# Kernel optimization log

Measured on AMD Instinct MI355X. Metric: run time of the kernel, lower is better.

The kernel has to match this reference:

```python
import jax, jax.numpy as jnp
import numpy as np

B, T, C, H = 8, 1024, 768, 12
D = C // H  # head_dim = 64


def setup_inputs() -> dict:
    key = jax.random.key(0)
    ks = jax.random.split(key, 5)
    return {
        "x": jax.random.normal(ks[0], (B, T, C), dtype=jnp.float32),
        "W_in": jax.random.normal(ks[1], (C, 3 * C), dtype=jnp.float32) * 0.02,
        "b_in": jax.random.normal(ks[2], (3 * C,), dtype=jnp.float32) * 0.02,
        "W_out": jax.random.normal(ks[3], (C, C), dtype=jnp.float32) * 0.02,
        "b_out": jax.random.normal(ks[4], (C,), dtype=jnp.float32) * 0.02,
    }


def reference(x, W_in, b_in, W_out, b_out):
    b, t, c = x.shape
    qkv = x @ W_in + b_in                       # [b, t, 3c]
    # NOTE: original code splits as (k, q, v) -- k first!
    k, q, v = jnp.split(qkv, 3, axis=2)
    # [b, h, t, d]
    k = k.reshape(b, t, H, D).transpose(0, 2, 1, 3)
    q = q.reshape(b, t, H, D).transpose(0, 2, 1, 3)
    v = v.reshape(b, t, H, D).transpose(0, 2, 1, 3)
    # NOTE: original applies NO 1/sqrt(d) scaling.
    scores = jnp.einsum("bhqd,bhkd->bhqk", q, k)
    causal = jnp.tril(jnp.ones((t, t), dtype=bool))
    scores = jnp.where(causal[None, None], scores, -jnp.inf)
    attn = jax.nn.softmax(scores, axis=-1)
    y = jnp.einsum("bhqk,bhkd->bhqd", attn, v)  # [b, h, t, d]
    y = y.transpose(0, 2, 1, 3).reshape(b, t, c)
    return y @ W_out + b_out
```

## Files before the change

kernel.cpp:

```cpp
#include <hip/hip_runtime.h>
#include <hip/hip_bf16.h>
#include <stdint.h>


typedef __bf16 bf16;
typedef __attribute__((ext_vector_type(4))) __bf16 bf16x4;
typedef __attribute__((ext_vector_type(8))) __bf16 bf16x8;
typedef __attribute__((ext_vector_type(4))) float f32x4;

#define NB 8
#define NT 1024
#define NC 768
#define NH 12
#define ND 64
#define NM (NB*NT)
#define N3C (3*NC)

typedef __attribute__((address_space(1))) void as1_void;
typedef __attribute__((address_space(3))) void as3_void;

__device__ __forceinline__ void gload_lds16(const void* g, void* l) {
  __builtin_amdgcn_global_load_lds((as1_void*)g, (as3_void*)l, 16, 0, 0);
}

__global__ void k_convert(const float* __restrict__ src, bf16* __restrict__ dst, int n4) {
  int i = blockIdx.x * blockDim.x + threadIdx.x;
  if (i < n4) {
    float4 v = reinterpret_cast<const float4*>(src)[i];
    bf16x4 o = { (bf16)v.x, (bf16)v.y, (bf16)v.z, (bf16)v.w };
    reinterpret_cast<bf16x4*>(dst)[i] = o;
  }
}

__global__ void k_transpose_w(const float* __restrict__ src, bf16* __restrict__ dst,
                              int R, int C) {
  __shared__ float tile[32][33];
  const int c0 = blockIdx.x * 32, r0 = blockIdx.y * 32;
  const int tx = threadIdx.x & 31, ty = threadIdx.x >> 5;
#pragma unroll
  for (int i = 0; i < 4; i++)
    tile[ty + i*8][tx] = src[(size_t)(r0 + ty + i*8) * C + c0 + tx];
  __syncthreads();
#pragma unroll
  for (int i = 0; i < 4; i++)
    dst[(size_t)(c0 + ty + i*8) * R + r0 + tx] = (bf16)tile[tx][ty + i*8];
}

template<bool OUT_BF16>
__global__ void k_gemm_bt(const bf16* __restrict__ A, const bf16* __restrict__ Bt,
                          const float* __restrict__ bias, void* __restrict__ Cout,
                          int M, int N, int K) {
  __shared__ __align__(16) bf16 As[128*32];
  __shared__ __align__(16) bf16 Bs[128*32];
  const int tm = blockIdx.x * 128, tn = blockIdx.y * 128;
  const int tid = threadIdx.x, lane = tid & 63, w = tid >> 6;
  const int wr = w >> 1, wc = w & 1;
  const int lr = lane & 15, lhi = lane >> 4;
  const int srow = tid >> 2, scol = (tid & 3) * 8;

  f32x4 acc[4][4];
#pragma unroll
  for (int m = 0; m < 4; m++)
#pragma unroll
    for (int n = 0; n < 4; n++) acc[m][n] = (f32x4){0.f, 0.f, 0.f, 0.f};

  for (int kt = 0; kt < K; kt += 32) {
    __syncthreads();
#pragma unroll
    for (int ch = 0; ch < 2; ch++) {
      gload_lds16(A + (size_t)(tm + ch*64 + srow) * K + kt + scol,
                  (char*)As + ch*4096 + tid*16);
      gload_lds16(Bt + (size_t)(tn + ch*64 + srow) * K + kt + scol,
                  (char*)Bs + ch*4096 + tid*16);
    }
    __syncthreads();

    bf16x8 af[4], bfr[4];
#pragma unroll
    for (int m = 0; m < 4; m++)
      af[m] = *reinterpret_cast<const bf16x8*>(
          (const char*)As + (wr*64 + m*16 + lr) * 64 + lhi * 16);
#pragma unroll
    for (int n = 0; n < 4; n++)
      bfr[n] = *reinterpret_cast<const bf16x8*>(
          (const char*)Bs + (wc*64 + n*16 + lr) * 64 + lhi * 16);
#pragma unroll
    for (int m = 0; m < 4; m++)
#pragma unroll
      for (int n = 0; n < 4; n++)
        acc[m][n] = __builtin_amdgcn_mfma_f32_16x16x32_bf16(af[m], bfr[n], acc[m][n], 0, 0, 0);
  }

#pragma unroll
  for (int m = 0; m < 4; m++)
#pragma unroll
    for (int n = 0; n < 4; n++) {
      const int col = tn + wc*64 + n*16 + lr;
      const float bv = bias[col];
#pragma unroll
      for (int j = 0; j < 4; j++) {
        const int row = tm + wr*64 + m*16 + lhi*4 + j;
        const float v = acc[m][n][j] + bv;
        if (OUT_BF16) ((bf16*)Cout)[(size_t)row * N + col] = (bf16)v;
        else          ((float*)Cout)[(size_t)row * N + col] = v;
      }
    }
}

__global__ void k_make_vt(const bf16* __restrict__ qkv, bf16* __restrict__ vt) {
  const int bh = blockIdx.x, b = bh / NH, h = bh % NH;
  const int t0 = blockIdx.y * 64;
  __shared__ bf16 tile[64][72];
  const int tx = threadIdx.x & 15, ty = threadIdx.x >> 4;
#pragma unroll
  for (int i = 0; i < 4; i++) {
    const int t = ty + i*16;
    bf16x4 v = *reinterpret_cast<const bf16x4*>(
        qkv + (size_t)(b*NT + t0 + t) * N3C + 2*NC + h*ND + tx*4);
#pragma unroll
    for (int j = 0; j < 4; j++) tile[t][tx*4 + j] = v[j];
  }
  __syncthreads();
#pragma unroll
  for (int i = 0; i < 4; i++) {
    const int d = ty + i*16;
    bf16x4 v;
#pragma unroll
    for (int j = 0; j < 4; j++) v[j] = tile[tx*4 + j][d];
    *reinterpret_cast<bf16x4*>(vt + ((size_t)bh*ND + d) * NT + t0 + tx*4) = v;
  }
}

__global__ void __launch_bounds__(64)
k_attn(const bf16* __restrict__ qkv, const bf16* __restrict__ vt,
       bf16* __restrict__ y) {
  const int bh = blockIdx.x, b = bh / NH, h = bh % NH;
  const int qt = (gridDim.y - 1) - blockIdx.y;
  const int lane = threadIdx.x;
  const int lr = lane & 15, lhi = lane >> 4;
  const int qbase = qt * 32;
  __shared__ __align__(16) bf16 P[32][68];

  bf16x8 qf[2][2];
#pragma unroll
  for (int m = 0; m < 2; m++)
#pragma unroll
    for (int kk = 0; kk < 2; kk++)
      qf[m][kk] = *reinterpret_cast<const bf16x8*>(
          qkv + (size_t)(b*NT + qbase + m*16 + lr) * N3C + NC + h*ND + kk*32 + lhi*8);

  f32x4 O[2][4];
  float L[2][4];
#pragma unroll
  for (int m = 0; m < 2; m++) {
#pragma unroll
    for (int d = 0; d < 4; d++) O[m][d] = (f32x4){0.f, 0.f, 0.f, 0.f};
#pragma unroll
    for (int j = 0; j < 4; j++) L[m][j] = 0.f;
  }

  const int nkb = (qbase >> 6) + 1;
  for (int kb = 0; kb < nkb; kb++) {
    const int k0 = kb * 64;
    f32x4 S[2][4];
#pragma unroll
    for (int m = 0; m < 2; m++)
#pragma unroll
      for (int g = 0; g < 4; g++) S[m][g] = (f32x4){0.f, 0.f, 0.f, 0.f};

#pragma unroll
    for (int g = 0; g < 4; g++) {
      const bf16* kp = qkv + (size_t)(b*NT + k0 + g*16 + lr) * N3C + h*ND;
      bf16x8 kf0 = *reinterpret_cast<const bf16x8*>(kp + lhi*8);
      bf16x8 kf1 = *reinterpret_cast<const bf16x8*>(kp + 32 + lhi*8);
#pragma unroll
      for (int m = 0; m < 2; m++) {
        S[m][g] = __builtin_amdgcn_mfma_f32_16x16x32_bf16(qf[m][0], kf0, S[m][g], 0, 0, 0);
        S[m][g] = __builtin_amdgcn_mfma_f32_16x16x32_bf16(qf[m][1], kf1, S[m][g], 0, 0, 0);
      }
    }

    bf16x8 vf[4][2];
#pragma unroll
    for (int dg = 0; dg < 4; dg++)
#pragma unroll
      for (int kk = 0; kk < 2; kk++)
        vf[dg][kk] = *reinterpret_cast<const bf16x8*>(
            vt + ((size_t)bh*ND + dg*16 + lr) * NT + k0 + kk*32 + lhi*8);

    const bool need_mask = (kb == nkb - 1);
#pragma unroll
    for (int m = 0; m < 2; m++)
#pragma unroll
      for (int g = 0; g < 4; g++) {
        const int key = k0 + g*16 + lr;
#pragma unroll
        for (int j = 0; j < 4; j++) {
          float s = S[m][g][j];
          if (need_mask) {
            const int row = qbase + m*16 + lhi*4 + j;
            if (key > row) s = -1e30f;
          }
          const float p = __expf(s);
          L[m][j] += p;
          P[m*16 + lhi*4 + j][g*16 + lr] = (bf16)p;
        }
      }

#pragma unroll
    for (int m = 0; m < 2; m++) {
#pragma unroll
      for (int kk = 0; kk < 2; kk++) {
        bf16x8 pf = *reinterpret_cast<const bf16x8*>(&P[m*16 + lr][kk*32 + lhi*8]);
#pragma unroll
        for (int dg = 0; dg < 4; dg++)
          O[m][dg] = __builtin_amdgcn_mfma_f32_16x16x32_bf16(pf, vf[dg][kk], O[m][dg], 0, 0, 0);
      }
    }
  }

#pragma unroll
  for (int m = 0; m < 2; m++)
#pragma unroll
    for (int j = 0; j < 4; j++) {
      float l = L[m][j];
      l += __shfl_xor(l, 1);
      l += __shfl_xor(l, 2);
      l += __shfl_xor(l, 4);
      l += __shfl_xor(l, 8);
      L[m][j] = 1.0f / l;
    }

#pragma unroll
  for (int m = 0; m < 2; m++)
#pragma unroll
    for (int dg = 0; dg < 4; dg++)
#pragma unroll
      for (int j = 0; j < 4; j++) {
        const int row = qbase + m*16 + lhi*4 + j;
        const int col = h*ND + dg*16 + lr;
        y[(size_t)(b*NT + row) * NC + col] = (bf16)(O[m][dg][j] * L[m][j]);
      }
}

extern "C" void kernel_launch(void* const* d_in, const int* in_sizes, int n_in,
                              void* d_out, int out_size, void* d_ws, size_t ws_size,
                              hipStream_t stream) {
  const float* x     = (const float*)d_in[0];
  const float* W_in  = (const float*)d_in[1];
  const float* b_in  = (const float*)d_in[2];
  const float* W_out = (const float*)d_in[3];
  const float* b_out = (const float*)d_in[4];
  float* out = (float*)d_out;
  char* ws = (char*)d_ws;

  bf16* xb  = (bf16*)(ws + 0);
  bf16* Wit = (bf16*)(ws + 12582912);
  bf16* Wot = (bf16*)(ws + 16121856);
  bf16* qkv = (bf16*)(ws + 17301504);
  bf16* vt  = (bf16*)(ws + 55050240);

  k_convert<<<6144, 256, 0, stream>>>(x, xb, NM * NC / 4);
  k_transpose_w<<<dim3(N3C/32, NC/32), 256, 0, stream>>>(W_in, Wit, NC, N3C);
  k_transpose_w<<<dim3(NC/32, NC/32), 256, 0, stream>>>(W_out, Wot, NC, NC);

  k_gemm_bt<true><<<dim3(NM/128, N3C/128), 256, 0, stream>>>(
      xb, Wit, b_in, qkv, NM, N3C, NC);

  k_make_vt<<<dim3(NB*NH, NT/64), 256, 0, stream>>>(qkv, vt);

  k_attn<<<dim3(NB*NH, NT/32), 64, 0, stream>>>(qkv, vt, xb );

  k_gemm_bt<false><<<dim3(NM/128, NC/128), 256, 0, stream>>>(
      xb, Wot, b_out, out, NM, NC, NC);
}
```

Before: 215.4 us.

## Split attention key blocks across four waves and pair causal query tiles per block

```diff
diff --git a/kernel.cpp b/kernel.cpp
--- a/kernel.cpp
+++ b/kernel.cpp
@@ -131,116 +131,144 @@
   }
 }
 
-__global__ void __launch_bounds__(64)
+__global__ void __launch_bounds__(256, 4)
 k_attn(const bf16* __restrict__ qkv, const bf16* __restrict__ vt,
        bf16* __restrict__ y) {
   const int bh = blockIdx.x, b = bh / NH, h = bh % NH;
-  const int qt = (gridDim.y - 1) - blockIdx.y;
-  const int lane = threadIdx.x;
+  const int p = blockIdx.y;
+  const int tid = threadIdx.x, w = tid >> 6, lane = tid & 63;
   const int lr = lane & 15, lhi = lane >> 4;
-  const int qbase = qt * 32;
-  __shared__ __align__(16) bf16 P[32][68];
-
-  bf16x8 qf[2][2];
-#pragma unroll
-  for (int m = 0; m < 2; m++)
-#pragma unroll
-    for (int kk = 0; kk < 2; kk++)
-      qf[m][kk] = *reinterpret_cast<const bf16x8*>(
-          qkv + (size_t)(b*NT + qbase + m*16 + lr) * N3C + NC + h*ND + kk*32 + lhi*8);
-
-  f32x4 O[2][4];
-  float L[2][4];
-#pragma unroll
-  for (int m = 0; m < 2; m++) {
-#pragma unroll
-    for (int d = 0; d < 4; d++) O[m][d] = (f32x4){0.f, 0.f, 0.f, 0.f};
-#pragma unroll
-    for (int j = 0; j < 4; j++) L[m][j] = 0.f;
-  }
-
-  const int nkb = (qbase >> 6) + 1;
-  for (int kb = 0; kb < nkb; kb++) {
-    const int k0 = kb * 64;
-    f32x4 S[2][4];
+
+  __shared__ __align__(16) bf16 P[4][32][68];
+  __shared__ __align__(16) float Obuf[2][32][68];
+  __shared__ float Lbuf[2][32];
+
+  for (int i = tid; i < 2*32*68; i += 256) ((float*)Obuf)[i] = 0.f;
+  if (tid < 64) ((float*)Lbuf)[tid] = 0.f;
+  __syncthreads();
+
+#pragma unroll 1
+  for (int tile = 0; tile < 2; tile++) {
+    const int qt = tile ? (31 - p) : p;
+    const int qbase = qt * 32;
+    const int nkb = (qbase >> 6) + 1;
+
+    bf16x8 qf[2][2];
 #pragma unroll
     for (int m = 0; m < 2; m++)
 #pragma unroll
-      for (int g = 0; g < 4; g++) S[m][g] = (f32x4){0.f, 0.f, 0.f, 0.f};
-
-#pragma unroll
-    for (int g = 0; g < 4; g++) {
-      const bf16* kp = qkv + (size_t)(b*NT + k0 + g*16 + lr) * N3C + h*ND;
-      bf16x8 kf0 = *reinterpret_cast<const bf16x8*>(kp + lhi*8);
-      bf16x8 kf1 = *reinterpret_cast<const bf16x8*>(kp + 32 + lhi*8);
-#pragma unroll
-      for (int m = 0; m < 2; m++) {
-        S[m][g] = __builtin_amdgcn_mfma_f32_16x16x32_bf16(qf[m][0], kf0, S[m][g], 0, 0, 0);
-        S[m][g] = __builtin_amdgcn_mfma_f32_16x16x32_bf16(qf[m][1], kf1, S[m][g], 0, 0, 0);
-      }
-    }
-
-    bf16x8 vf[4][2];
-#pragma unroll
-    for (int dg = 0; dg < 4; dg++)
-#pragma unroll
       for (int kk = 0; kk < 2; kk++)
-        vf[dg][kk] = *reinterpret_cast<const bf16x8*>(
-            vt + ((size_t)bh*ND + dg*16 + lr) * NT + k0 + kk*32 + lhi*8);
-
-    const bool need_mask = (kb == nkb - 1);
-#pragma unroll
-    for (int m = 0; m < 2; m++)
+        qf[m][kk] = *reinterpret_cast<const bf16x8*>(
+            qkv + (size_t)(b*NT + qbase + m*16 + lr) * N3C + NC + h*ND + kk*32 + lhi*8);
+
+    f32x4 O[2][4];
+    float L[2][4];
+#pragma unroll
+    for (int m = 0; m < 2; m++) {
+#pragma unroll
+      for (int d = 0; d < 4; d++) O[m][d] = (f32x4){0.f, 0.f, 0.f, 0.f};
+#pragma unroll
+      for (int j = 0; j < 4; j++) L[m][j] = 0.f;
+    }
+
+    for (int kb = w; kb < nkb; kb += 4) {
+      const int k0 = kb * 64;
+      f32x4 S[2][4];
+#pragma unroll
+      for (int m = 0; m < 2; m++)
+#pragma unroll
+        for (int g = 0; g < 4; g++) S[m][g] = (f32x4){0.f, 0.f, 0.f, 0.f};
+
 #pragma unroll
       for (int g = 0; g < 4; g++) {
-        const int key = k0 + g*16 + lr;
-#pragma unroll
-        for (int j = 0; j < 4; j++) {
-          float s = S[m][g][j];
-          if (need_mask) {
-            const int row = qbase + m*16 + lhi*4 + j;
-            if (key > row) s = -1e30f;
-          }
-          const float p = __expf(s);
-          L[m][j] += p;
-          P[m*16 + lhi*4 + j][g*16 + lr] = (bf16)p;
+        const bf16* kp = qkv + (size_t)(b*NT + k0 + g*16 + lr) * N3C + h*ND;
+        bf16x8 kf0 = *reinterpret_cast<const bf16x8*>(kp + lhi*8);
+        bf16x8 kf1 = *reinterpret_cast<const bf16x8*>(kp + 32 + lhi*8);
+#pragma unroll
+        for (int m = 0; m < 2; m++) {
+          S[m][g] = __builtin_amdgcn_mfma_f32_16x16x32_bf16(qf[m][0], kf0, S[m][g], 0, 0, 0);
+          S[m][g] = __builtin_amdgcn_mfma_f32_16x16x32_bf16(qf[m][1], kf1, S[m][g], 0, 0, 0);
         }
       }
 
-#pragma unroll
-    for (int m = 0; m < 2; m++) {
-#pragma unroll
-      for (int kk = 0; kk < 2; kk++) {
-        bf16x8 pf = *reinterpret_cast<const bf16x8*>(&P[m*16 + lr][kk*32 + lhi*8]);
-#pragma unroll
-        for (int dg = 0; dg < 4; dg++)
-          O[m][dg] = __builtin_amdgcn_mfma_f32_16x16x32_bf16(pf, vf[dg][kk], O[m][dg], 0, 0, 0);
+      bf16x8 vf[4][2];
+#pragma unroll
+      for (int dg = 0; dg < 4; dg++)
+#pragma unroll
+        for (int kk = 0; kk < 2; kk++)
+          vf[dg][kk] = *reinterpret_cast<const bf16x8*>(
+              vt + ((size_t)bh*ND + dg*16 + lr) * NT + k0 + kk*32 + lhi*8);
+
+      const bool need_mask = (kb == nkb - 1);
+#pragma unroll
+      for (int m = 0; m < 2; m++)
+#pragma unroll
+        for (int g = 0; g < 4; g++) {
+          const int key = k0 + g*16 + lr;
+#pragma unroll
+          for (int j = 0; j < 4; j++) {
+            float s = S[m][g][j];
+            if (need_mask) {
+              const int row = qbase + m*16 + lhi*4 + j;
+              if (key > row) s = -1e30f;
+            }
+            const float ppv = __expf(s);
+            L[m][j] += ppv;
+            P[w][m*16 + lhi*4 + j][g*16 + lr] = (bf16)ppv;
+          }
+        }
+
+#pragma unroll
+      for (int m = 0; m < 2; m++) {
+#pragma unroll
+        for (int kk = 0; kk < 2; kk++) {
+          bf16x8 pf = *reinterpret_cast<const bf16x8*>(&P[w][m*16 + lr][kk*32 + lhi*8]);
+#pragma unroll
+          for (int dg = 0; dg < 4; dg++)
+            O[m][dg] = __builtin_amdgcn_mfma_f32_16x16x32_bf16(pf, vf[dg][kk], O[m][dg], 0, 0, 0);
+        }
       }
     }
-  }
-
-#pragma unroll
-  for (int m = 0; m < 2; m++)
-#pragma unroll
-    for (int j = 0; j < 4; j++) {
-      float l = L[m][j];
-      l += __shfl_xor(l, 1);
-      l += __shfl_xor(l, 2);
-      l += __shfl_xor(l, 4);
-      l += __shfl_xor(l, 8);
-      L[m][j] = 1.0f / l;
-    }
-
-#pragma unroll
-  for (int m = 0; m < 2; m++)
-#pragma unroll
-    for (int dg = 0; dg < 4; dg++)
+
+#pragma unroll
+    for (int m = 0; m < 2; m++)
 #pragma unroll
       for (int j = 0; j < 4; j++) {
-        const int row = qbase + m*16 + lhi*4 + j;
-        const int col = h*ND + dg*16 + lr;
-        y[(size_t)(b*NT + row) * NC + col] = (bf16)(O[m][dg][j] * L[m][j]);
+        float l = L[m][j];
+        l += __shfl_xor(l, 1);
+        l += __shfl_xor(l, 2);
+        l += __shfl_xor(l, 4);
+        l += __shfl_xor(l, 8);
+        L[m][j] = l;
       }
+
+#pragma unroll
+    for (int m = 0; m < 2; m++)
+#pragma unroll
+      for (int dg = 0; dg < 4; dg++)
+#pragma unroll
+        for (int j = 0; j < 4; j++)
+          atomicAdd(&Obuf[tile][m*16 + lhi*4 + j][dg*16 + lr], O[m][dg][j]);
+    if (lr == 0)
+#pragma unroll
+      for (int m = 0; m < 2; m++)
+#pragma unroll
+        for (int j = 0; j < 4; j++)
+          atomicAdd(&Lbuf[tile][m*16 + lhi*4 + j], L[m][j]);
+
+    __syncthreads();
+
+    {
+      const int q = tid >> 3, dvb = (tid & 7) * 8;
+      const float invl = 1.0f / Lbuf[tile][q];
+      bf16x8 ov;
+#pragma unroll
+      for (int i = 0; i < 8; i++)
+        ov[i] = (bf16)(Obuf[tile][q][dvb + i] * invl);
+      *reinterpret_cast<bf16x8*>(
+          y + (size_t)(b*NT + qbase + q) * NC + h*ND + dvb) = ov;
+    }
+  }
 }
 
 extern "C" void kernel_launch(void* const* d_in, const int* in_sizes, int n_in,
@@ -269,7 +297,7 @@
 
   k_make_vt<<<dim3(NB*NH, NT/64), 256, 0, stream>>>(qkv, vt);
 
-  k_attn<<<dim3(NB*NH, NT/32), 64, 0, stream>>>(qkv, vt, xb );
+  k_attn<<<dim3(NB*NH, 16), 256, 0, stream>>>(qkv, vt, xb );
 
   k_gemm_bt<false><<<dim3(NM/128, NC/128), 256, 0, stream>>>(
       xb, Wot, b_out, out, NM, NC, NC);
```

Measured after the change: 335.3 us. 1.56x slower.

## Pair causal query tiles per block and double-buffer K fragment loads

Applied to the files above, without the earlier changes.

```diff
diff --git a/kernel.cpp b/kernel.cpp
--- a/kernel.cpp
+++ b/kernel.cpp
@@ -131,116 +131,144 @@
   }
 }
 
-__global__ void __launch_bounds__(64)
-k_attn(const bf16* __restrict__ qkv, const bf16* __restrict__ vt,
-       bf16* __restrict__ y) {
+__global__ void k_attn(const bf16* __restrict__ qkv, const bf16* __restrict__ vt,
+                       bf16* __restrict__ y) {
   const int bh = blockIdx.x, b = bh / NH, h = bh % NH;
-  const int qt = (gridDim.y - 1) - blockIdx.y;
+  const int p = blockIdx.y;
   const int lane = threadIdx.x;
   const int lr = lane & 15, lhi = lane >> 4;
-  const int qbase = qt * 32;
   __shared__ __align__(16) bf16 P[32][68];
 
-  bf16x8 qf[2][2];
-#pragma unroll
-  for (int m = 0; m < 2; m++)
-#pragma unroll
-    for (int kk = 0; kk < 2; kk++)
-      qf[m][kk] = *reinterpret_cast<const bf16x8*>(
-          qkv + (size_t)(b*NT + qbase + m*16 + lr) * N3C + NC + h*ND + kk*32 + lhi*8);
-
-  f32x4 O[2][4];
-  float L[2][4];
-#pragma unroll
-  for (int m = 0; m < 2; m++) {
-#pragma unroll
-    for (int d = 0; d < 4; d++) O[m][d] = (f32x4){0.f, 0.f, 0.f, 0.f};
-#pragma unroll
-    for (int j = 0; j < 4; j++) L[m][j] = 0.f;
-  }
-
-  const int nkb = (qbase >> 6) + 1;
-  for (int kb = 0; kb < nkb; kb++) {
-    const int k0 = kb * 64;
-    f32x4 S[2][4];
+#define LOAD_K(DST, K0)                                                        \
+  {                                                                            \
+    _Pragma("unroll")                                                          \
+    for (int g = 0; g < 4; g++) {                                              \
+      const bf16* kp = qkv + (size_t)(b*NT + (K0) + g*16 + lr) * N3C + h*ND;   \
+      DST[g][0] = *reinterpret_cast<const bf16x8*>(kp + lhi*8);                \
+      DST[g][1] = *reinterpret_cast<const bf16x8*>(kp + 32 + lhi*8);           \
+    }                                                                          \
+  }
+
+#define ATTN_STEP(KCUR, KNXT, KB)                                              \
+  {                                                                            \
+    const int k0 = (KB) * 64;                                                  \
+    const int kn = ((KB) + 1 < nkb) ? k0 + 64 : k0;                            \
+                             \
+    bf16x8 vf[4][2];                                                           \
+    _Pragma("unroll")                                                          \
+    for (int dg = 0; dg < 4; dg++)                                             \
+      _Pragma("unroll")                                                        \
+      for (int kk = 0; kk < 2; kk++)                                           \
+        vf[dg][kk] = *reinterpret_cast<const bf16x8*>(                         \
+            vt + ((size_t)bh*ND + dg*16 + lr) * NT + k0 + kk*32 + lhi*8);      \
+                   \
+    LOAD_K(KNXT, kn);                                                          \
+    f32x4 S[2][4];                                                             \
+    _Pragma("unroll")                                                          \
+    for (int m = 0; m < 2; m++)                                                \
+      _Pragma("unroll")                                                        \
+      for (int g = 0; g < 4; g++) S[m][g] = (f32x4){0.f, 0.f, 0.f, 0.f};       \
+    _Pragma("unroll")                                                          \
+    for (int g = 0; g < 4; g++)                                                \
+      _Pragma("unroll")                                                        \
+      for (int m = 0; m < 2; m++) {                                            \
+        S[m][g] = __builtin_amdgcn_mfma_f32_16x16x32_bf16(qf[m][0], KCUR[g][0],\
+                                                          S[m][g], 0, 0, 0);   \
+        S[m][g] = __builtin_amdgcn_mfma_f32_16x16x32_bf16(qf[m][1], KCUR[g][1],\
+                                                          S[m][g], 0, 0, 0);   \
+      }                                                                        \
+    const bool need_mask = ((KB) == nkb - 1);                                  \
+    _Pragma("unroll")                                                          \
+    for (int m = 0; m < 2; m++)                                                \
+      _Pragma("unroll")                                                        \
+      for (int g = 0; g < 4; g++) {                                            \
+        const int key = k0 + g*16 + lr;                                        \
+        _Pragma("unroll")                                                      \
+        for (int j = 0; j < 4; j++) {                                          \
+          float s = S[m][g][j];                                                \
+          if (need_mask) {                                                     \
+            const int row = qbase + m*16 + lhi*4 + j;                          \
+            if (key > row) s = -1e30f;                                         \
+          }                                                                    \
+          const float ppv = __expf(s);   \
+          L[m][j] += ppv;                                                      \
+          P[m*16 + lhi*4 + j][g*16 + lr] = (bf16)ppv;                          \
+        }                                                                      \
+      }                                                                        \
+    _Pragma("unroll")                                                          \
+    for (int m = 0; m < 2; m++)                                                \
+      _Pragma("unroll")                                                        \
+      for (int kk = 0; kk < 2; kk++) {                                         \
+        bf16x8 pf = *reinterpret_cast<const bf16x8*>(&P[m*16 + lr][kk*32 + lhi*8]); \
+        _Pragma("unroll")                                                      \
+        for (int dg = 0; dg < 4; dg++)                                         \
+          O[m][dg] = __builtin_amdgcn_mfma_f32_16x16x32_bf16(pf, vf[dg][kk],   \
+                                                             O[m][dg], 0, 0, 0); \
+      }                                                                        \
+  }
+
+#pragma unroll 1
+  for (int half = 0; half < 2; half++) {
+    const int qt = half ? (31 - p) : p;
+    const int qbase = qt * 32;
+    const int nkb = (qbase >> 6) + 1;
+
+    bf16x8 qf[2][2];
 #pragma unroll
     for (int m = 0; m < 2; m++)
 #pragma unroll
-      for (int g = 0; g < 4; g++) S[m][g] = (f32x4){0.f, 0.f, 0.f, 0.f};
-
-#pragma unroll
-    for (int g = 0; g < 4; g++) {
-      const bf16* kp = qkv + (size_t)(b*NT + k0 + g*16 + lr) * N3C + h*ND;
-      bf16x8 kf0 = *reinterpret_cast<const bf16x8*>(kp + lhi*8);
-      bf16x8 kf1 = *reinterpret_cast<const bf16x8*>(kp + 32 + lhi*8);
-#pragma unroll
-      for (int m = 0; m < 2; m++) {
-        S[m][g] = __builtin_amdgcn_mfma_f32_16x16x32_bf16(qf[m][0], kf0, S[m][g], 0, 0, 0);
-        S[m][g] = __builtin_amdgcn_mfma_f32_16x16x32_bf16(qf[m][1], kf1, S[m][g], 0, 0, 0);
+      for (int kk = 0; kk < 2; kk++)
+        qf[m][kk] = *reinterpret_cast<const bf16x8*>(
+            qkv + (size_t)(b*NT + qbase + m*16 + lr) * N3C + NC + h*ND + kk*32 + lhi*8);
+
+    f32x4 O[2][4];
+    float L[2][4];
+#pragma unroll
+    for (int m = 0; m < 2; m++) {
+#pragma unroll
+      for (int d = 0; d < 4; d++) O[m][d] = (f32x4){0.f, 0.f, 0.f, 0.f};
+#pragma unroll
+      for (int j = 0; j < 4; j++) L[m][j] = 0.f;
+    }
+
+    bf16x8 kfA[4][2], kfB[4][2];
+    LOAD_K(kfA, 0);
+    int kb = 0;
+#pragma unroll 1
+    while (true) {
+      ATTN_STEP(kfA, kfB, kb);
+      kb++;
+      if (kb >= nkb) break;
+      ATTN_STEP(kfB, kfA, kb);
+      kb++;
+      if (kb >= nkb) break;
+    }
+
+#pragma unroll
+    for (int m = 0; m < 2; m++)
+#pragma unroll
+      for (int j = 0; j < 4; j++) {
+        float l = L[m][j];
+        l += __shfl_xor(l, 1);
+        l += __shfl_xor(l, 2);
+        l += __shfl_xor(l, 4);
+        l += __shfl_xor(l, 8);
+        L[m][j] = 1.0f / l;
       }
-    }
-
-    bf16x8 vf[4][2];
-#pragma unroll
-    for (int dg = 0; dg < 4; dg++)
-#pragma unroll
-      for (int kk = 0; kk < 2; kk++)
-        vf[dg][kk] = *reinterpret_cast<const bf16x8*>(
-            vt + ((size_t)bh*ND + dg*16 + lr) * NT + k0 + kk*32 + lhi*8);
-
-    const bool need_mask = (kb == nkb - 1);
+
 #pragma unroll
     for (int m = 0; m < 2; m++)
 #pragma unroll
-      for (int g = 0; g < 4; g++) {
-        const int key = k0 + g*16 + lr;
+      for (int dg = 0; dg < 4; dg++)
 #pragma unroll
         for (int j = 0; j < 4; j++) {
-          float s = S[m][g][j];
-          if (need_mask) {
-            const int row = qbase + m*16 + lhi*4 + j;
-            if (key > row) s = -1e30f;
-          }
-          const float p = __expf(s);
-          L[m][j] += p;
-          P[m*16 + lhi*4 + j][g*16 + lr] = (bf16)p;
+          const int row = qbase + m*16 + lhi*4 + j;
+          const int col = h*ND + dg*16 + lr;
+          y[(size_t)(b*NT + row) * NC + col] = (bf16)(O[m][dg][j] * L[m][j]);
         }
-      }
-
-#pragma unroll
-    for (int m = 0; m < 2; m++) {
-#pragma unroll
-      for (int kk = 0; kk < 2; kk++) {
-        bf16x8 pf = *reinterpret_cast<const bf16x8*>(&P[m*16 + lr][kk*32 + lhi*8]);
-#pragma unroll
-        for (int dg = 0; dg < 4; dg++)
-          O[m][dg] = __builtin_amdgcn_mfma_f32_16x16x32_bf16(pf, vf[dg][kk], O[m][dg], 0, 0, 0);
-      }
-    }
-  }
-
-#pragma unroll
-  for (int m = 0; m < 2; m++)
-#pragma unroll
-    for (int j = 0; j < 4; j++) {
-      float l = L[m][j];
-      l += __shfl_xor(l, 1);
-      l += __shfl_xor(l, 2);
-      l += __shfl_xor(l, 4);
-      l += __shfl_xor(l, 8);
-      L[m][j] = 1.0f / l;
-    }
-
-#pragma unroll
-  for (int m = 0; m < 2; m++)
-#pragma unroll
-    for (int dg = 0; dg < 4; dg++)
-#pragma unroll
-      for (int j = 0; j < 4; j++) {
-        const int row = qbase + m*16 + lhi*4 + j;
-        const int col = h*ND + dg*16 + lr;
-        y[(size_t)(b*NT + row) * NC + col] = (bf16)(O[m][dg][j] * L[m][j]);
-      }
+  }
+#undef ATTN_STEP
+#undef LOAD_K
 }
 
 extern "C" void kernel_launch(void* const* d_in, const int* in_sizes, int n_in,
@@ -269,7 +297,7 @@
 
   k_make_vt<<<dim3(NB*NH, NT/64), 256, 0, stream>>>(qkv, vt);
 
-  k_attn<<<dim3(NB*NH, NT/32), 64, 0, stream>>>(qkv, vt, xb );
+  k_attn<<<dim3(NB*NH, 16), 64, 0, stream>>>(qkv, vt, xb );
 
   k_gemm_bt<false><<<dim3(NM/128, NC/128), 256, 0, stream>>>(
       xb, Wot, b_out, out, NM, NC, NC);
```

After: 316.5 us. 1.47x slower.
